# Kernel optimization log

Measured on AMD Instinct MI355X. Metric: run time of the kernel, lower is better.

The kernel has to match this reference:

```python
import jax, jax.numpy as jnp
import numpy as np
import itertools

VOXEL_SIZE = np.array([0.05, 0.05, 0.1], np.float32)   # xyz, from cfg.voxel_size
GRID_OFFSET = np.array([0.0, -40.0, -3.0], np.float32)  # xyz, cfg.grid_bounds[:3]
BN_EPS = 1e-3

# ---------------- rulebook construction (numpy, mirrors spconv indice pairs) ----------------

def _enc(c, shape):
    Z, Y, X = shape
    c = c.astype(np.int64)
    return ((c[:, 0] * Z + c[:, 1]) * Y + c[:, 2]) * X + c[:, 3]

def _lookup(sk, order, q):
    pos = np.clip(np.searchsorted(sk, q), 0, len(sk) - 1)
    return np.where((q >= 0) & (sk[pos] == q), order[pos], -1).astype(np.int32)

def _subm_rulebook(coords, shape):
    # submanifold conv k=3, pad=1: output sites == input sites; neighbor = out + (k-1)
    keys = _enc(coords, shape)
    order = np.argsort(keys).astype(np.int32)
    sk = keys[order]
    dims = np.array(shape)
    rows = []
    for off in itertools.product((-1, 0, 1), repeat=3):
        nb = coords[:, 1:] + np.array(off)
        inb = ((nb >= 0) & (nb < dims)).all(1)
        full = np.concatenate([coords[:, :1], nb], 1)
        q = np.where(inb, _enc(full, shape), -1)
        rows.append(_lookup(sk, order, q))
    return np.stack(rows)  # [27, N] input index or -1

def _strided_rulebook(coords, shape_in, ksize, stride, pad):
    # regular sparse conv: out active = any site receiving a contribution; in = out*s - p + k
    ksize = np.array(ksize); stride = np.array(stride); pad = np.array(pad)
    shape_out = tuple((((np.array(shape_in) + 2 * pad - ksize) // stride) + 1).tolist())
    keys = _enc(coords, shape_in)
    order = np.argsort(keys).astype(np.int32)
    sk = keys[order]
    cand = []
    for k in itertools.product(*[range(int(x)) for x in ksize]):
        num = coords[:, 1:] + pad - np.array(k)
        ok = (num % stride == 0).all(1)
        o = num // stride
        ok &= (o >= 0).all(1) & (o < np.array(shape_out)).all(1)
        cand.append(np.concatenate([coords[ok, :1], o[ok]], 1))
    out_coords = np.unique(np.concatenate(cand, 0), axis=0).astype(np.int32)
    dims_in = np.array(shape_in)
    rows = []
    for k in itertools.product(*[range(int(x)) for x in ksize]):
        ic = out_coords[:, 1:] * stride - pad + np.array(k)
        inb = ((ic >= 0) & (ic < dims_in)).all(1)
        full = np.concatenate([out_coords[:, :1], ic], 1)
        q = np.where(inb, _enc(full, shape_in), -1)
        rows.append(_lookup(sk, order, q))
    return out_coords, np.stack(rows), shape_out

# ---------------- inputs ----------------

def setup_inputs() -> dict:
    rng = np.random.default_rng(0)
    B, NPB = 2, 8000
    shape0 = (41, 1600, 1280)
    parts = []
    for b in range(B):
        c = np.stack([rng.integers(0, shape0[0], 4 * NPB),
                      rng.integers(0, shape0[1], 4 * NPB),
                      rng.integers(0, shape0[2], 4 * NPB)], 1)
        c = np.unique(c, axis=0)[:NPB]
        parts.append(np.concatenate([np.full((len(c), 1), b), c], 1))
    coords0 = np.concatenate(parts, 0).astype(np.int32)

    rb0 = _subm_rulebook(coords0, shape0)
    coords1, rbc1, shape1 = _strided_rulebook(coords0, shape0, (3, 3, 3), (2, 2, 2), (1, 1, 1))
    rb1 = _subm_rulebook(coords1, shape1)
    coords2, rbc2, shape2 = _strided_rulebook(coords1, shape1, (3, 3, 3), (2, 2, 2), (1, 1, 1))
    rb2 = _subm_rulebook(coords2, shape2)
    coords3, rbc3, shape3 = _strided_rulebook(coords2, shape2, (3, 3, 3), (2, 2, 2), (0, 1, 1))
    rb3 = _subm_rulebook(coords3, shape3)
    coords4, rbc4, shape4 = _strided_rulebook(coords3, shape3, (3, 1, 1), (2, 1, 1), (0, 0, 0))

    def w(*s):
        return jnp.asarray((rng.standard_normal(s) * 0.1).astype(np.float32))

    inp = {"features": jnp.asarray(rng.standard_normal((len(coords0), 4)).astype(np.float32))}
    specs = [("1a", 27, 4, 16), ("1b", 27, 16, 16), ("1c", 27, 16, 32),
             ("2a", 27, 32, 32), ("2b", 27, 32, 32), ("2c", 27, 32, 64),
             ("3a", 27, 64, 64), ("3b", 27, 64, 64), ("3c", 27, 64, 64), ("3d", 27, 64, 64),
             ("4a", 27, 64, 64), ("4b", 27, 64, 64), ("4c", 27, 64, 64), ("4d", 3, 64, 64)]
    for name, K, ci, co in specs:
        inp["w" + name] = w(K, ci, co)
        inp["g" + name] = jnp.asarray((np.abs(rng.standard_normal(co)) + 0.5).astype(np.float32))
        inp["b" + name] = jnp.asarray((rng.standard_normal(co) * 0.1).astype(np.float32))
    inp.update(coordinates=jnp.asarray(coords0), coords1=jnp.asarray(coords1),
               coords2=jnp.asarray(coords2), coords3=jnp.asarray(coords3),
               rb0=jnp.asarray(rb0), rbc1=jnp.asarray(rbc1), rb1=jnp.asarray(rb1),
               rbc2=jnp.asarray(rbc2), rb2=jnp.asarray(rb2), rbc3=jnp.asarray(rbc3),
               rb3=jnp.asarray(rb3), rbc4=jnp.asarray(rbc4), batch_size=B)
    return inp

# ---------------- forward math ----------------

def _sconv(feat, rb, W):
    # gather-GEMM-scatter: rb[k,n] = input row feeding output n via kernel offset k (-1 = none)
    out = jnp.zeros((rb.shape[1], W.shape[2]), feat.dtype)
    for k in range(W.shape[0]):
        idx = rb[k]
        g = jnp.where(idx[:, None] >= 0, feat[jnp.clip(idx, 0)], 0.0)
        out = out + g @ W[k]
    return out

def _bn_relu(x, g, b):
    # BatchNorm1d in training mode over active voxels (biased var), eps=1e-3, then ReLU
    m = jnp.mean(x, 0)
    v = jnp.mean(jnp.square(x - m), 0)
    return jax.nn.relu((x - m) * (g / jnp.sqrt(v + BN_EPS)) + b)

def reference(features, w1a, g1a, b1a, w1b, g1b, b1b, w1c, g1c, b1c,
              w2a, g2a, b2a, w2b, g2b, b2b, w2c, g2c, b2c,
              w3a, g3a, b3a, w3b, g3b, b3b, w3c, g3c, b3c, w3d, g3d, b3d,
              w4a, g4a, b4a, w4b, g4b, b4b, w4c, g4c, b4c, w4d, g4d, b4d,
              coordinates, coords1, coords2, coords3,
              rb0, rbc1, rb1, rbc2, rb2, rbc3, rb3, rbc4, batch_size):
    f0 = features
    h = _bn_relu(_sconv(f0, rb0, w1a), g1a, b1a)
    h = _bn_relu(_sconv(h, rb0, w1b), g1b, b1b)
    f1 = _bn_relu(_sconv(h, rbc1, w1c), g1c, b1c)
    h = _bn_relu(_sconv(f1, rb1, w2a), g2a, b2a)
    h = _bn_relu(_sconv(h, rb1, w2b), g2b, b2b)
    f2 = _bn_relu(_sconv(h, rbc2, w2c), g2c, b2c)
    h = _bn_relu(_sconv(f2, rb2, w3a), g3a, b3a)
    h = _bn_relu(_sconv(h, rb2, w3b), g3b, b3b)
    h = _bn_relu(_sconv(h, rb2, w3c), g3c, b3c)
    f3 = _bn_relu(_sconv(h, rbc3, w3d), g3d, b3d)
    h = _bn_relu(_sconv(f3, rb3, w4a), g4a, b4a)
    h = _bn_relu(_sconv(h, rb3, w4b), g4b, b4b)
    h = _bn_relu(_sconv(h, rb3, w4c), g4c, b4c)
    f4 = _bn_relu(_sconv(h, rbc4, w4d), g4d, b4d)

    vs = jnp.asarray(VOXEL_SIZE)
    off = jnp.asarray(GRID_OFFSET)
    def to_global(stride, c):
        # indices are (b,z,y,x); flip -> (x,y,z,b); take xyz
        return jnp.flip(c, 1)[:, :3].astype(jnp.float32) * (vs * stride) + off
    xyz0 = to_global(1, coordinates)
    xyz1 = to_global(2, coords1)
    xyz2 = to_global(4, coords2)
    xyz3 = to_global(8, coords3)
    return (xyz0, f0, xyz1, f1, xyz2, f2, xyz3, f3, f4)
```

## Files before the change

kernel.cpp:

```cpp
#include <hip/hip_runtime.h>

#define BN_EPS 1e-3f
#define NREP 16

typedef __attribute__((ext_vector_type(8))) short short8;
typedef __attribute__((ext_vector_type(4))) float float4v;

__device__ __forceinline__ short f2bf(float f) {
    unsigned u = __float_as_uint(f);
    unsigned r = (u + 0x7FFFu + ((u >> 16) & 1u)) >> 16;
    return (short)r;
}

template <int N>
__device__ __forceinline__ void waitcnt_vm() {
    __builtin_amdgcn_s_waitcnt(0xF70 | (N & 15) | ((N >> 4) << 14));
}


__global__ __launch_bounds__(256) void zero_kernel(float* p, int n) {
    int i = blockIdx.x * 256 + threadIdx.x;
    if (i < n) p[i] = 0.f;
}

__global__ __launch_bounds__(256) void copy_kernel(const float* __restrict__ in,
                                                   float* __restrict__ out, int n) {
    int i = blockIdx.x * 256 + threadIdx.x;
    if (i < n) out[i] = in[i];
}

__global__ __launch_bounds__(256) void zero_rows_kernel(short* a, short* b, long maxN) {
    int t = threadIdx.x;
    if (t < 32) a[maxN * 32 + t] = 0;
    else if (t < 96) a[maxN * 64 + (t - 32)] = 0;
    else if (t < 128) b[maxN * 32 + (t - 96)] = 0;
    else if (t < 192) b[maxN * 64 + (t - 128)] = 0;
}

__global__ __launch_bounds__(256) void xyz_kernel(const int* __restrict__ coords,
                                                  float* __restrict__ out, int N,
                                                  float sx, float sy, float sz) {
    int n = blockIdx.x * 256 + threadIdx.x;
    if (n >= N) return;
    int4 c = ((const int4*)coords)[n];
    out[n * 3 + 0] = c.w * sx;
    out[n * 3 + 1] = c.z * sy - 40.0f;
    out[n * 3 + 2] = c.y * sz - 3.0f;
}

__global__ __launch_bounds__(256) void convert_f0(const float* __restrict__ f,
                                                  short* __restrict__ dst, int N) {
    int i = blockIdx.x * 256 + threadIdx.x;
    if (i >= N * 32) return;
    int c = i & 31, n = i >> 5;
    dst[i] = (c < 4) ? f2bf(f[n * 4 + c]) : (short)0;
}

struct PrepAll {
    const float* src[14];
    short* dst[14];
    int CI[14];
    int CO[14];
    int CHP[14];
    int cum[15];
};

__global__ __launch_bounds__(256) void prep_all_kernel(PrepAll d) {
    int i = blockIdx.x * 256 + threadIdx.x;
    if (i >= d.cum[14]) return;
    int l = 0;
    while (l < 13 && i >= d.cum[l + 1]) ++l;
    int f = i - d.cum[l];
    int CO = d.CO[l], CI = d.CI[l];
    int NCH = d.CHP[l] / 32, CT = CO / 16;
    int e = f & 7;
    int u = f >> 3;
    int l16 = u & 15;
    int q = (u >> 4) & 3;
    int u2 = u >> 6;
    int t = u2 % CT;
    int c = (u2 / CT) % NCH;
    int k = u2 / (CT * NCH);
    int ci = c * 32 + q * 8 + e;
    int co = t * 16 + l16;
    float v = (ci < CI) ? d.src[l][((size_t)k * CI + ci) * CO + co] : 0.f;
    d.dst[l][f] = f2bf(v);
}

struct ASet {
    short8 v0, v1, v2, v3;
};

template <int CHP, int CO, int K>
__global__ __launch_bounds__(64, 3) void sconv_wav(const short* __restrict__ feat,
                                                   const int* __restrict__ rb,
                                                   const short* __restrict__ Wt,
                                                   float* __restrict__ out,
                                                   float* __restrict__ stats, int N, int zrow) {
    constexpr int NCH = CHP / 32;
    constexpr int CT = CO / 16;
    constexpr int BTILE = CO * CHP;
    constexpr int BF = NCH * CT;

    const int lane = threadIdx.x & 63;
    const int quad = lane >> 4;
    const int l16 = lane & 15;
    const int m0 = blockIdx.x * 32;

    const short* fquad = feat + quad * 8;

    const int r0 = m0 + l16;
    const int r1 = r0 + 16;
    const bool v0 = r0 < N;
    const bool v1 = r1 < N;
    const int* p0 = rb + (v0 ? r0 : 0);
    const int* p1 = rb + (v1 ? r1 : 0);

    auto loadRb = [&](int k) {
        int2 j;
        j.x = p0[(size_t)k * N];
        j.y = p1[(size_t)k * N];
        if (!v0) j.x = -1;
        if (!v1) j.y = -1;
        return j;
    };
    auto aliveOf = [&](int2 j) {
        return (__ballot(j.x >= 0) | __ballot(j.y >= 0)) != 0ull;
    };

    struct BSet {
        short8 f[BF];
    };
    auto loadB = [&](int k) {
        BSet b;
        const short* wk = Wt + (size_t)k * BTILE;
#pragma unroll
        for (int j = 0; j < BF; ++j)
            b.f[j] = *(const short8*)(wk + ((j * 64) + quad * 16 + l16) * 8);
        return b;
    };
    auto issueA = [&](int2 j) {
        ASet s;
        const short* q0 = fquad + (size_t)(j.x < 0 ? zrow : j.x) * CHP;
        const short* q1 = fquad + (size_t)(j.y < 0 ? zrow : j.y) * CHP;
        s.v0 = *(const short8*)q0;
        s.v2 = *(const short8*)q1;
        if constexpr (NCH == 2) {
            s.v1 = *(const short8*)(q0 + 32);
            s.v3 = *(const short8*)(q1 + 32);
        } else {
            s.v1 = (short8)0;
            s.v3 = (short8)0;
        }
        return s;
    };

    float4v acc[2][CT];
#pragma unroll
    for (int mt = 0; mt < 2; ++mt)
#pragma unroll
        for (int t = 0; t < CT; ++t) acc[mt][t] = (float4v)0.f;

    int2 t0 = loadRb(0);
    int2 t1 = loadRb(1);
    waitcnt_vm<0>();
    bool alA = aliveOf(t0);
    bool alB = aliveOf(t1);
    int2 qA, qB, qC;
    qA.x = qA.y = qB.x = qB.y = qC.x = qC.y = -1;
    if (K > 2) qA = loadRb(2);
    if (K > 3) qB = loadRb(3);
    ASet sA = issueA(t0);
    ASet sB = issueA(t1);
    ASet sC;
    bool alC = false;

#pragma unroll 1
    for (int i = 0; i < K; ++i) {
        BSet bCur = loadB(i);
        const bool haveRb = (i + 4 < K);
        if (haveRb) qC = loadRb(i + 4);
        if (haveRb) waitcnt_vm<2>();
        else waitcnt_vm<0>();
        if (i + 2 < K) {
            alC = aliveOf(qA);
            sC = issueA(qA);
        }
        if (alA) {
#pragma unroll
            for (int c = 0; c < NCH; ++c) {
#pragma unroll
                for (int t = 0; t < CT; ++t) {
                    short8 bf = bCur.f[c * CT + t];
#pragma unroll
                    for (int mt = 0; mt < 2; ++mt) {
                        short8 af = (mt == 0) ? ((c == 0) ? sA.v0 : sA.v1)
                                              : ((c == 0) ? sA.v2 : sA.v3);
                        acc[mt][t] =
                            __builtin_amdgcn_mfma_f32_16x16x32_bf16(af, bf, acc[mt][t], 0, 0, 0);
                    }
                }
            }
        }
        sA = sB;
        sB = sC;
        alA = alB;
        alB = alC;
        qA = qB;
        qB = qC;
    }

#pragma unroll
    for (int mt = 0; mt < 2; ++mt)
#pragma unroll
        for (int t = 0; t < CT; ++t) {
            int col = t * 16 + l16;
#pragma unroll
            for (int r = 0; r < 4; ++r) {
                int orow = m0 + mt * 16 + quad * 4 + r;
                if (orow < N) out[(size_t)orow * CO + col] = acc[mt][t][r];
            }
        }

    float* st = stats + (size_t)(blockIdx.x & (NREP - 1)) * 128;
#pragma unroll
    for (int t = 0; t < CT; ++t) {
        float s = 0.f, ss = 0.f;
#pragma unroll
        for (int mt = 0; mt < 2; ++mt)
#pragma unroll
            for (int r = 0; r < 4; ++r) {
                float v = acc[mt][t][r];
                s += v;
                ss += v * v;
            }
        s += __shfl_xor(s, 16);
        s += __shfl_xor(s, 32);
        ss += __shfl_xor(ss, 16);
        ss += __shfl_xor(ss, 32);
        if (lane < 16) {
            atomicAdd(&st[t * 16 + lane], s);
            atomicAdd(&st[64 + t * 16 + lane], ss);
        }
    }
}

template <int COUT, int CHPN, bool F32OUT, bool BFOUT>
__global__ __launch_bounds__(256) void bn_apply(const float* __restrict__ x,
                                                const float* __restrict__ stats,
                                                const float* __restrict__ g,
                                                const float* __restrict__ b,
                                                float* __restrict__ fout,
                                                short* __restrict__ bfout, int N) {
    constexpr int CW = BFOUT ? CHPN : COUT;
    constexpr int CV = CW / 8;
    __shared__ float ssc[COUT];
    __shared__ float ssh[COUT];
    int tid = threadIdx.x;
    if (tid < COUT) {
        float s = 0.f, q = 0.f;
#pragma unroll
        for (int r = 0; r < NREP; ++r) {
            s += stats[r * 128 + tid];
            q += stats[r * 128 + 64 + tid];
        }
        float inv = 1.0f / (float)N;
        float m = s * inv;
        float v = q * inv - m * m;
        float sc = g[tid] / sqrtf(v + BN_EPS);
        ssc[tid] = sc;
        ssh[tid] = b[tid] - m * sc;
    }
    __syncthreads();
    long i = (long)blockIdx.x * 256 + tid;
    if (i >= (long)N * CV) return;
    int c8 = (int)(i % CV);
    long n = i / CV;
    int cb = c8 * 8;
    float y[8];
#pragma unroll
    for (int j = 0; j < 8; ++j) y[j] = 0.f;
    if (cb < COUT) {
        const float4v* xr = (const float4v*)(x + n * COUT + cb);
        float4v a0 = xr[0];
        float4v a1 = xr[1];
#pragma unroll
        for (int j = 0; j < 4; ++j) {
            y[j] = fmaxf(a0[j] * ssc[cb + j] + ssh[cb + j], 0.f);
            y[4 + j] = fmaxf(a1[j] * ssc[cb + 4 + j] + ssh[cb + 4 + j], 0.f);
        }
        if constexpr (F32OUT) {
            float* fo = fout + n * COUT + cb;
            if ((((unsigned long long)fout) & 15ull) == 0) {
                float4v o0, o1;
#pragma unroll
                for (int j = 0; j < 4; ++j) {
                    o0[j] = y[j];
                    o1[j] = y[4 + j];
                }
                ((float4v*)fo)[0] = o0;
                ((float4v*)fo)[1] = o1;
            } else {
#pragma unroll
                for (int j = 0; j < 8; ++j) fo[j] = y[j];
            }
        }
    }
    if constexpr (BFOUT) {
        short8 p;
#pragma unroll
        for (int j = 0; j < 8; ++j) p[j] = f2bf(y[j]);
        *(short8*)(bfout + n * CHPN + cb) = p;
    }
}


template <int CHP, int CO, int K>
static void conv(const short* fin, const int* rb, const short* wt, float* preact, float* stats,
                 int N, int zrow, hipStream_t stream) {
    dim3 grid((N + 31) / 32);
    hipLaunchKernelGGL((sconv_wav<CHP, CO, K>), grid, dim3(64), 0, stream, fin, rb, wt, preact,
                       stats, N, zrow);
}

template <int COUT, int CHPN, bool F32OUT, bool BFOUT>
static void apply(const float* preact, const float* stats, const float* g, const float* b,
                  float* fout, short* bfout, int N, hipStream_t stream) {
    constexpr int CW = BFOUT ? CHPN : COUT;
    constexpr int CV = CW / 8;
    int blocks = (int)(((long)N * CV + 255) / 256);
    hipLaunchKernelGGL((bn_apply<COUT, CHPN, F32OUT, BFOUT>), dim3(blocks), dim3(256), 0, stream,
                       preact, stats, g, b, fout, bfout, N);
}

extern "C" void kernel_launch(void* const* d_in, const int* in_sizes, int n_in, void* d_out,
                              int out_size, void* d_ws, size_t ws_size, hipStream_t stream) {
    const float* features = (const float*)d_in[0];
    const float* W[14];
    const float* G[14];
    const float* Bb[14];
    for (int i = 0; i < 14; ++i) {
        W[i] = (const float*)d_in[1 + 3 * i];
        G[i] = (const float*)d_in[2 + 3 * i];
        Bb[i] = (const float*)d_in[3 + 3 * i];
    }
    const int* coords0 = (const int*)d_in[43];
    const int* coords1 = (const int*)d_in[44];
    const int* coords2 = (const int*)d_in[45];
    const int* coords3 = (const int*)d_in[46];
    const int* rb0 = (const int*)d_in[47];
    const int* rbc1 = (const int*)d_in[48];
    const int* rb1 = (const int*)d_in[49];
    const int* rbc2 = (const int*)d_in[50];
    const int* rb2 = (const int*)d_in[51];
    const int* rbc3 = (const int*)d_in[52];
    const int* rb3 = (const int*)d_in[53];
    const int* rbc4 = (const int*)d_in[54];

    const int N0 = in_sizes[0] / 4;
    const int N1 = in_sizes[44] / 4;
    const int N2 = in_sizes[45] / 4;
    const int N3 = in_sizes[46] / 4;
    const int N4 = in_sizes[54] / 3;

    float* out = (float*)d_out;
    long off = 0;
    float* xyz0 = out + off; off += (long)N0 * 3;
    float* f0   = out + off; off += (long)N0 * 4;
    float* xyz1 = out + off; off += (long)N1 * 3;
    float* f1   = out + off; off += (long)N1 * 32;
    float* xyz2 = out + off; off += (long)N2 * 3;
    float* f2   = out + off; off += (long)N2 * 64;
    float* xyz3 = out + off; off += (long)N3 * 3;
    float* f3   = out + off; off += (long)N3 * 64;
    float* f4   = out + off;

    long maxN = N0;
    if (N1 > maxN) maxN = N1;
    if (N2 > maxN) maxN = N2;
    if (N3 > maxN) maxN = N3;
    if (N4 > maxN) maxN = N4;
    const int zrow = (int)maxN;

    float* preact = (float*)d_ws;
    float* statsBase = preact + (size_t)maxN * 64;
    short* bfA = (short*)(statsBase + 14 * NREP * 128);
    short* bfB = bfA + (size_t)(maxN + 1) * 64;
    short* wtBase = bfB + (size_t)(maxN + 1) * 64;

    static const int KK[14] = {27, 27, 27, 27, 27, 27, 27, 27, 27, 27, 27, 27, 27, 3};
    static const int CI[14] = {4, 16, 16, 32, 32, 32, 64, 64, 64, 64, 64, 64, 64, 64};
    static const int CO[14] = {16, 16, 32, 32, 32, 64, 64, 64, 64, 64, 64, 64, 64, 64};
    short* WT[14];
    PrepAll pd;
    {
        size_t o = 0;
        int cum = 0;
        for (int l = 0; l < 14; ++l) {
            WT[l] = wtBase + o;
            int chp = CI[l] <= 32 ? 32 : 64;
            pd.src[l] = W[l];
            pd.dst[l] = WT[l];
            pd.CI[l] = CI[l];
            pd.CO[l] = CO[l];
            pd.CHP[l] = chp;
            pd.cum[l] = cum;
            cum += KK[l] * CO[l] * chp;
            o += (size_t)KK[l] * CO[l] * chp;
        }
        pd.cum[14] = cum;
    }

    int nstats = 14 * NREP * 128;
    hipLaunchKernelGGL(zero_kernel, dim3((nstats + 255) / 256), dim3(256), 0, stream, statsBase,
                       nstats);
    hipLaunchKernelGGL(zero_rows_kernel, dim3(1), dim3(256), 0, stream, bfA, bfB, maxN);
    hipLaunchKernelGGL(prep_all_kernel, dim3((pd.cum[14] + 255) / 256), dim3(256), 0, stream, pd);

    hipLaunchKernelGGL(copy_kernel, dim3((N0 * 4 + 255) / 256), dim3(256), 0, stream, features, f0,
                       N0 * 4);
    hipLaunchKernelGGL(xyz_kernel, dim3((N0 + 255) / 256), dim3(256), 0, stream, coords0, xyz0, N0,
                       0.05f, 0.05f, 0.1f);
    hipLaunchKernelGGL(xyz_kernel, dim3((N1 + 255) / 256), dim3(256), 0, stream, coords1, xyz1, N1,
                       0.1f, 0.1f, 0.2f);
    hipLaunchKernelGGL(xyz_kernel, dim3((N2 + 255) / 256), dim3(256), 0, stream, coords2, xyz2, N2,
                       0.2f, 0.2f, 0.4f);
    hipLaunchKernelGGL(xyz_kernel, dim3((N3 + 255) / 256), dim3(256), 0, stream, coords3, xyz3, N3,
                       0.4f, 0.4f, 0.8f);
    hipLaunchKernelGGL(convert_f0, dim3((N0 * 32 + 255) / 256), dim3(256), 0, stream, features,
                       bfA, N0);

    float* st = statsBase;
#define STAT(l) (st + (size_t)(l)*NREP * 128)

    conv<32, 16, 27>(bfA, rb0, WT[0], preact, STAT(0), N0, zrow, stream);
    apply<16, 32, false, true>(preact, STAT(0), G[0], Bb[0], nullptr, bfB, N0, stream);
    conv<32, 16, 27>(bfB, rb0, WT[1], preact, STAT(1), N0, zrow, stream);
    apply<16, 32, false, true>(preact, STAT(1), G[1], Bb[1], nullptr, bfA, N0, stream);
    conv<32, 32, 27>(bfA, rbc1, WT[2], preact, STAT(2), N1, zrow, stream);
    apply<32, 32, true, true>(preact, STAT(2), G[2], Bb[2], f1, bfB, N1, stream);

    conv<32, 32, 27>(bfB, rb1, WT[3], preact, STAT(3), N1, zrow, stream);
    apply<32, 32, false, true>(preact, STAT(3), G[3], Bb[3], nullptr, bfA, N1, stream);
    conv<32, 32, 27>(bfA, rb1, WT[4], preact, STAT(4), N1, zrow, stream);
    apply<32, 32, false, true>(preact, STAT(4), G[4], Bb[4], nullptr, bfB, N1, stream);
    conv<32, 64, 27>(bfB, rbc2, WT[5], preact, STAT(5), N2, zrow, stream);
    apply<64, 64, true, true>(preact, STAT(5), G[5], Bb[5], f2, bfA, N2, stream);

    conv<64, 64, 27>(bfA, rb2, WT[6], preact, STAT(6), N2, zrow, stream);
    apply<64, 64, false, true>(preact, STAT(6), G[6], Bb[6], nullptr, bfB, N2, stream);
    conv<64, 64, 27>(bfB, rb2, WT[7], preact, STAT(7), N2, zrow, stream);
    apply<64, 64, false, true>(preact, STAT(7), G[7], Bb[7], nullptr, bfA, N2, stream);
    conv<64, 64, 27>(bfA, rb2, WT[8], preact, STAT(8), N2, zrow, stream);
    apply<64, 64, false, true>(preact, STAT(8), G[8], Bb[8], nullptr, bfB, N2, stream);
    conv<64, 64, 27>(bfB, rbc3, WT[9], preact, STAT(9), N3, zrow, stream);
    apply<64, 64, true, true>(preact, STAT(9), G[9], Bb[9], f3, bfA, N3, stream);

    conv<64, 64, 27>(bfA, rb3, WT[10], preact, STAT(10), N3, zrow, stream);
    apply<64, 64, false, true>(preact, STAT(10), G[10], Bb[10], nullptr, bfB, N3, stream);
    conv<64, 64, 27>(bfB, rb3, WT[11], preact, STAT(11), N3, zrow, stream);
    apply<64, 64, false, true>(preact, STAT(11), G[11], Bb[11], nullptr, bfA, N3, stream);
    conv<64, 64, 27>(bfA, rb3, WT[12], preact, STAT(12), N3, zrow, stream);
    apply<64, 64, false, true>(preact, STAT(12), G[12], Bb[12], nullptr, bfB, N3, stream);
    conv<64, 64, 3>(bfB, rbc4, WT[13], preact, STAT(13), N4, zrow, stream);
    apply<64, 64, true, false>(preact, STAT(13), G[13], Bb[13], f4, nullptr, N4, stream);
#undef STAT
}
```

Measured before the change: 688.2 us.

## Deepen sparse-conv prefetch pipeline and pack four waves per block

The sparse convolution kernel now prefetches weight tiles two offsets ahead and gathered features three offsets ahead, using computed vmcnt wait thresholds instead of loading B synchronously each iteration. Blocks grow from one wave to four, each wave handling its own 32-row tile, and launch bounds change accordingly. The aim is to hide global memory latency for the gather and weight loads. The cost is more live registers for the extra buffered sets, which may reduce occupancy. The hand-derived wait counts also have to match the exact number of outstanding loads to stay correct.

Result: slower. 750.7 us (+9.1%).

```diff
diff --git a/kernel.cpp b/kernel.cpp
--- a/kernel.cpp
+++ b/kernel.cpp
@@ -92,7 +92,7 @@
 };
 
 template <int CHP, int CO, int K>
-__global__ __launch_bounds__(64, 3) void sconv_wav(const short* __restrict__ feat,
+__global__ __launch_bounds__(256, 2) void sconv_dp(const short* __restrict__ feat,
                                                    const int* __restrict__ rb,
                                                    const short* __restrict__ Wt,
                                                    float* __restrict__ out,
@@ -100,12 +100,20 @@
     constexpr int NCH = CHP / 32;
     constexpr int CT = CO / 16;
     constexpr int BTILE = CO * CHP;
-    constexpr int BF = NCH * CT;
-
-    const int lane = threadIdx.x & 63;
+    constexpr int BF = BTILE / 512;
+    constexpr int A_ = 2 * NCH;
+    constexpr int WS = 2 * (A_ + BF) + 4;
+    constexpr int WM = 2 * (A_ + BF) + 2;
+    constexpr int W2 = 2 * (A_ + BF);
+    constexpr int W1 = A_ + BF;
+
+    const int tid = threadIdx.x;
+    const int w = tid >> 6;
+    const int lane = tid & 63;
     const int quad = lane >> 4;
     const int l16 = lane & 15;
-    const int m0 = blockIdx.x * 32;
+    const int tile = blockIdx.x * 4 + w;
+    const int m0 = tile * 32;
 
     const short* fquad = feat + quad * 8;
 
@@ -162,36 +170,50 @@
         for (int t = 0; t < CT; ++t) acc[mt][t] = (float4v)0.f;
 
     int2 t0 = loadRb(0);
-    int2 t1 = loadRb(1);
+    int2 t1, t2;
+    t1.x = t1.y = t2.x = t2.y = -1;
+    if (K > 1) t1 = loadRb(1);
+    if (K > 2) t2 = loadRb(2);
     waitcnt_vm<0>();
     bool alA = aliveOf(t0);
-    bool alB = aliveOf(t1);
+    bool alB = (K > 1) ? aliveOf(t1) : false;
+    bool alC = (K > 2) ? aliveOf(t2) : false;
+    bool alD = false;
+
+    BSet bA = loadB(0), bB, bC;
+    ASet sA = issueA(t0), sB, sC, sD;
+    if (K > 1) {
+        bB = loadB(1);
+        sB = issueA(t1);
+    }
+    if (K > 2) sC = issueA(t2);
     int2 qA, qB, qC;
     qA.x = qA.y = qB.x = qB.y = qC.x = qC.y = -1;
-    if (K > 2) qA = loadRb(2);
-    if (K > 3) qB = loadRb(3);
-    ASet sA = issueA(t0);
-    ASet sB = issueA(t1);
-    ASet sC;
-    bool alC = false;
+    if (K > 3) qA = loadRb(3);
+    if (K > 4) qB = loadRb(4);
 
 #pragma unroll 1
     for (int i = 0; i < K; ++i) {
-        BSet bCur = loadB(i);
-        const bool haveRb = (i + 4 < K);
-        if (haveRb) qC = loadRb(i + 4);
-        if (haveRb) waitcnt_vm<2>();
+        if (i + 2 < K) bC = loadB(i + 2);
+        if (i + 5 < K) qC = loadRb(i + 5);
+        const int d = K - 1 - i;
+        if (d >= 5) waitcnt_vm<WS>();
+        else if (d == 4) waitcnt_vm<WM>();
+        else if (d >= 2) waitcnt_vm<W2>();
+        else if (d == 1) waitcnt_vm<W1>();
         else waitcnt_vm<0>();
-        if (i + 2 < K) {
-            alC = aliveOf(qA);
-            sC = issueA(qA);
+        if (i + 3 < K) {
+            alD = aliveOf(qA);
+            sD = issueA(qA);
+        } else {
+            alD = false;
         }
         if (alA) {
 #pragma unroll
             for (int c = 0; c < NCH; ++c) {
 #pragma unroll
                 for (int t = 0; t < CT; ++t) {
-                    short8 bf = bCur.f[c * CT + t];
+                    short8 bf = bA.f[c * CT + t];
 #pragma unroll
                     for (int mt = 0; mt < 2; ++mt) {
                         short8 af = (mt == 0) ? ((c == 0) ? sA.v0 : sA.v1)
@@ -202,10 +224,14 @@
                 }
             }
         }
+        bA = bB;
+        bB = bC;
         sA = sB;
         sB = sC;
+        sC = sD;
         alA = alB;
         alB = alC;
+        alC = alD;
         qA = qB;
         qB = qC;
     }
@@ -222,7 +248,7 @@
             }
         }
 
-    float* st = stats + (size_t)(blockIdx.x & (NREP - 1)) * 128;
+    float* st = stats + (size_t)(tile & (NREP - 1)) * 128;
 #pragma unroll
     for (int t = 0; t < CT; ++t) {
         float s = 0.f, ss = 0.f;
@@ -318,8 +344,8 @@
 template <int CHP, int CO, int K>
 static void conv(const short* fin, const int* rb, const short* wt, float* preact, float* stats,
                  int N, int zrow, hipStream_t stream) {
-    dim3 grid((N + 31) / 32);
-    hipLaunchKernelGGL((sconv_wav<CHP, CO, K>), grid, dim3(64), 0, stream, fin, rb, wt, preact,
+    dim3 grid((N + 127) / 128);
+    hipLaunchKernelGGL((sconv_dp<CHP, CO, K>), grid, dim3(256), 0, stream, fin, rb, wt, preact,
                        stats, N, zrow);
 }
 
```

## Compact active kernel offsets in LDS, prefetch weights, store bf16 preactivations

Applied to the files above, without the earlier changes.

The conv kernel now loads the whole rulebook tile for the block into shared memory and builds a list of kernel offsets that have any active neighbor. It loops only over those offsets, prefetching both weight and feature fragments one or two steps ahead with explicit vmcnt waits. The preactivation buffer is stored as bf16 instead of fp32, which halves its write and read traffic in the BN-apply pass. The cost is lower precision in the stored preactivations, while BN statistics are still taken from fp32 accumulators. Occupancy drops to 2 waves per SIMD in exchange for more registers.

Result: faster. 649.9 us (median of 2 runs) (-5.6%).

```diff
diff --git a/kernel.cpp b/kernel.cpp
--- a/kernel.cpp
+++ b/kernel.cpp
@@ -10,6 +10,10 @@
     unsigned u = __float_as_uint(f);
     unsigned r = (u + 0x7FFFu + ((u >> 16) & 1u)) >> 16;
     return (short)r;
+}
+
+__device__ __forceinline__ float bf2f(short s) {
+    return __uint_as_float(((unsigned)(unsigned short)s) << 16);
 }
 
 template <int N>
@@ -92,57 +96,69 @@
 };
 
 template <int CHP, int CO, int K>
-__global__ __launch_bounds__(64, 3) void sconv_wav(const short* __restrict__ feat,
-                                                   const int* __restrict__ rb,
-                                                   const short* __restrict__ Wt,
-                                                   float* __restrict__ out,
-                                                   float* __restrict__ stats, int N, int zrow) {
+__global__ __launch_bounds__(64, 2) void sconv_wc(const short* __restrict__ feat,
+                                                  const int* __restrict__ rb,
+                                                  const short* __restrict__ Wt,
+                                                  short* __restrict__ out,
+                                                  float* __restrict__ stats, int N, int zrow) {
     constexpr int NCH = CHP / 32;
     constexpr int CT = CO / 16;
     constexpr int BTILE = CO * CHP;
-    constexpr int BF = NCH * CT;
+    constexpr int BF = BTILE / 512;
+    constexpr int A_ = 2 * NCH;
+    constexpr int DB = (BF >= 8) ? 1 : 2;
+    constexpr int WN2 = 2 * (BF + A_);
+    constexpr int WN1 = BF + A_;
+    constexpr int WD2 = 2 * A_ + BF;
+    constexpr int WD1 = A_ + BF;
+
+    __shared__ int sIdx[K * 32];
+    __shared__ int sFlag[K];
+    __shared__ int sKl[K];
+    __shared__ int sKn;
 
     const int lane = threadIdx.x & 63;
     const int quad = lane >> 4;
     const int l16 = lane & 15;
     const int m0 = blockIdx.x * 32;
 
+    if (lane < K) sFlag[lane] = 0;
+    __syncthreads();
+    for (int e = lane; e < K * 32; e += 64) {
+        int r = m0 + (e & 31);
+        int v = (r < N) ? rb[(size_t)(e >> 5) * N + r] : -1;
+        sIdx[e] = v;
+        if (v >= 0) sFlag[e >> 5] = 1;
+    }
+    __syncthreads();
+    {
+        int f = (lane < K) ? sFlag[lane] : 0;
+        unsigned long long m = __ballot(f != 0);
+        if (f) sKl[__popcll(m & ((1ull << lane) - 1ull))] = lane;
+        if (lane == 0) sKn = (int)__popcll(m);
+    }
+    __syncthreads();
+    const int nk = sKn;
+
     const short* fquad = feat + quad * 8;
-
-    const int r0 = m0 + l16;
-    const int r1 = r0 + 16;
-    const bool v0 = r0 < N;
-    const bool v1 = r1 < N;
-    const int* p0 = rb + (v0 ? r0 : 0);
-    const int* p1 = rb + (v1 ? r1 : 0);
-
-    auto loadRb = [&](int k) {
-        int2 j;
-        j.x = p0[(size_t)k * N];
-        j.y = p1[(size_t)k * N];
-        if (!v0) j.x = -1;
-        if (!v1) j.y = -1;
-        return j;
-    };
-    auto aliveOf = [&](int2 j) {
-        return (__ballot(j.x >= 0) | __ballot(j.y >= 0)) != 0ull;
-    };
 
     struct BSet {
         short8 f[BF];
     };
-    auto loadB = [&](int k) {
+    auto issueB = [&](int kp) {
         BSet b;
-        const short* wk = Wt + (size_t)k * BTILE;
+        const short* wk = Wt + (size_t)kp * BTILE;
 #pragma unroll
         for (int j = 0; j < BF; ++j)
             b.f[j] = *(const short8*)(wk + ((j * 64) + quad * 16 + l16) * 8);
         return b;
     };
-    auto issueA = [&](int2 j) {
+    auto issueA = [&](int kp) {
         ASet s;
-        const short* q0 = fquad + (size_t)(j.x < 0 ? zrow : j.x) * CHP;
-        const short* q1 = fquad + (size_t)(j.y < 0 ? zrow : j.y) * CHP;
+        int i0 = sIdx[kp * 32 + l16];
+        int i1 = sIdx[kp * 32 + 16 + l16];
+        const short* q0 = fquad + (size_t)(i0 < 0 ? zrow : i0) * CHP;
+        const short* q1 = fquad + (size_t)(i1 < 0 ? zrow : i1) * CHP;
         s.v0 = *(const short8*)q0;
         s.v2 = *(const short8*)q1;
         if constexpr (NCH == 2) {
@@ -161,53 +177,55 @@
 #pragma unroll
         for (int t = 0; t < CT; ++t) acc[mt][t] = (float4v)0.f;
 
-    int2 t0 = loadRb(0);
-    int2 t1 = loadRb(1);
-    waitcnt_vm<0>();
-    bool alA = aliveOf(t0);
-    bool alB = aliveOf(t1);
-    int2 qA, qB, qC;
-    qA.x = qA.y = qB.x = qB.y = qC.x = qC.y = -1;
-    if (K > 2) qA = loadRb(2);
-    if (K > 3) qB = loadRb(3);
-    ASet sA = issueA(t0);
-    ASet sB = issueA(t1);
-    ASet sC;
-    bool alC = false;
+    BSet bA{}, bB{}, bC{};
+    ASet sA{}, sB{}, sC{};
+    if (nk > 0) {
+        bA = issueB(sKl[0]);
+        sA = issueA(sKl[0]);
+    }
+    if (DB == 2 && nk > 1) bB = issueB(sKl[1]);
+    if (nk > 1) sB = issueA(sKl[1]);
 
 #pragma unroll 1
-    for (int i = 0; i < K; ++i) {
-        BSet bCur = loadB(i);
-        const bool haveRb = (i + 4 < K);
-        if (haveRb) qC = loadRb(i + 4);
-        if (haveRb) waitcnt_vm<2>();
-        else waitcnt_vm<0>();
-        if (i + 2 < K) {
-            alC = aliveOf(qA);
-            sC = issueA(qA);
-        }
-        if (alA) {
-#pragma unroll
-            for (int c = 0; c < NCH; ++c) {
-#pragma unroll
-                for (int t = 0; t < CT; ++t) {
-                    short8 bf = bCur.f[c * CT + t];
-#pragma unroll
-                    for (int mt = 0; mt < 2; ++mt) {
-                        short8 af = (mt == 0) ? ((c == 0) ? sA.v0 : sA.v1)
-                                              : ((c == 0) ? sA.v2 : sA.v3);
-                        acc[mt][t] =
-                            __builtin_amdgcn_mfma_f32_16x16x32_bf16(af, bf, acc[mt][t], 0, 0, 0);
-                    }
+    for (int i = 0; i < nk; ++i) {
+        if constexpr (DB == 2) {
+            if (i + 2 < nk) bC = issueB(sKl[i + 2]);
+        } else {
+            if (i + 1 < nk) bB = issueB(sKl[i + 1]);
+        }
+        if (i + 2 < nk) sC = issueA(sKl[i + 2]);
+        const int d = nk - 1 - i;
+        if constexpr (DB == 2) {
+            if (d >= 2) waitcnt_vm<WN2>();
+            else if (d == 1) waitcnt_vm<WN1>();
+            else waitcnt_vm<0>();
+        } else {
+            if (d >= 2) waitcnt_vm<WD2>();
+            else if (d == 1) waitcnt_vm<WD1>();
+            else waitcnt_vm<0>();
+        }
+#pragma unroll
+        for (int c = 0; c < NCH; ++c) {
+#pragma unroll
+            for (int t = 0; t < CT; ++t) {
+                short8 bf = bA.f[c * CT + t];
+#pragma unroll
+                for (int mt = 0; mt < 2; ++mt) {
+                    short8 af = (mt == 0) ? ((c == 0) ? sA.v0 : sA.v1)
+                                          : ((c == 0) ? sA.v2 : sA.v3);
+                    acc[mt][t] =
+                        __builtin_amdgcn_mfma_f32_16x16x32_bf16(af, bf, acc[mt][t], 0, 0, 0);
                 }
             }
         }
+        if constexpr (DB == 2) {
+            bA = bB;
+            bB = bC;
+        } else {
+            bA = bB;
+        }
         sA = sB;
         sB = sC;
-        alA = alB;
-        alB = alC;
-        qA = qB;
-        qB = qC;
     }
 
 #pragma unroll
@@ -218,7 +236,7 @@
 #pragma unroll
             for (int r = 0; r < 4; ++r) {
                 int orow = m0 + mt * 16 + quad * 4 + r;
-                if (orow < N) out[(size_t)orow * CO + col] = acc[mt][t][r];
+                if (orow < N) out[(size_t)orow * CO + col] = f2bf(acc[mt][t][r]);
             }
         }
 
@@ -246,7 +264,7 @@
 }
 
 template <int COUT, int CHPN, bool F32OUT, bool BFOUT>
-__global__ __launch_bounds__(256) void bn_apply(const float* __restrict__ x,
+__global__ __launch_bounds__(256) void bn_apply(const short* __restrict__ x,
                                                 const float* __restrict__ stats,
                                                 const float* __restrict__ g,
                                                 const float* __restrict__ b,
@@ -281,14 +299,10 @@
 #pragma unroll
     for (int j = 0; j < 8; ++j) y[j] = 0.f;
     if (cb < COUT) {
-        const float4v* xr = (const float4v*)(x + n * COUT + cb);
-        float4v a0 = xr[0];
-        float4v a1 = xr[1];
-#pragma unroll
-        for (int j = 0; j < 4; ++j) {
-            y[j] = fmaxf(a0[j] * ssc[cb + j] + ssh[cb + j], 0.f);
-            y[4 + j] = fmaxf(a1[j] * ssc[cb + 4 + j] + ssh[cb + 4 + j], 0.f);
-        }
+        short8 xv = *(const short8*)(x + n * COUT + cb);
+#pragma unroll
+        for (int j = 0; j < 8; ++j)
+            y[j] = fmaxf(bf2f(xv[j]) * ssc[cb + j] + ssh[cb + j], 0.f);
         if constexpr (F32OUT) {
             float* fo = fout + n * COUT + cb;
             if ((((unsigned long long)fout) & 15ull) == 0) {
@@ -316,15 +330,15 @@
 
 
 template <int CHP, int CO, int K>
-static void conv(const short* fin, const int* rb, const short* wt, float* preact, float* stats,
+static void conv(const short* fin, const int* rb, const short* wt, short* preact, float* stats,
                  int N, int zrow, hipStream_t stream) {
     dim3 grid((N + 31) / 32);
-    hipLaunchKernelGGL((sconv_wav<CHP, CO, K>), grid, dim3(64), 0, stream, fin, rb, wt, preact,
+    hipLaunchKernelGGL((sconv_wc<CHP, CO, K>), grid, dim3(64), 0, stream, fin, rb, wt, preact,
                        stats, N, zrow);
 }
 
 template <int COUT, int CHPN, bool F32OUT, bool BFOUT>
-static void apply(const float* preact, const float* stats, const float* g, const float* b,
+static void apply(const short* preact, const float* stats, const float* g, const float* b,
                   float* fout, short* bfout, int N, hipStream_t stream) {
     constexpr int CW = BFOUT ? CHPN : COUT;
     constexpr int CV = CW / 8;
@@ -382,8 +396,8 @@
     if (N4 > maxN) maxN = N4;
     const int zrow = (int)maxN;
 
-    float* preact = (float*)d_ws;
-    float* statsBase = preact + (size_t)maxN * 64;
+    short* preact = (short*)d_ws;
+    float* statsBase = (float*)(preact + (size_t)maxN * 64);
     short* bfA = (short*)(statsBase + 14 * NREP * 128);
     short* bfB = bfA + (size_t)(maxN + 1) * 64;
     short* wtBase = bfB + (size_t)(maxN + 1) * 64;
```
